# Kernel tuning notes

Hardware: AMD Instinct MI355X
Metric: run time of the kernel (lower is better)

Reference implementation:

```python
import jax, jax.numpy as jnp
import numpy as np
from jax import lax


def _conv(x, w, b):
    # x: [B,C,H,W], w: [O,I,3,3] (OIHW), SAME padding, stride 1
    y = lax.conv_general_dilated(x, w, (1, 1), 'SAME',
                                 dimension_numbers=('NCHW', 'OIHW', 'NCHW'))
    return y + b[None, :, None, None]


def _maxpool2(x):
    return lax.reduce_window(x, -jnp.inf, lax.max, (1, 1, 2, 2), (1, 1, 2, 2), 'VALID')


def setup_inputs() -> dict:
    key = jax.random.key(0)
    ks = iter(jax.random.split(key, 40))

    def conv_w(o, i):
        std = np.sqrt(2.0 / (9.0 * o)).astype(np.float32)  # kaiming as in _initialize_weights
        return jax.random.normal(next(ks), (o, i, 3, 3), jnp.float32) * std

    def lin_w(o, i):
        return jax.random.normal(next(ks), (o, i), jnp.float32) * 0.01

    inp = {
        'x': jax.random.normal(next(ks), (64, 3, 64, 64), jnp.float32),
        'y': jax.random.randint(next(ks), (64,), 0, 1000, dtype=jnp.int32),
        'b_table': jax.random.randint(next(ks), (1000, 128), 0, 512, dtype=jnp.int32),
        'cw0': conv_w(64, 3),    'cb0': jnp.zeros((64,), jnp.float32),
        'cw1': conv_w(128, 64),  'cb1': jnp.zeros((128,), jnp.float32),
        'cw2a': conv_w(256, 128), 'cb2a': jnp.zeros((256,), jnp.float32),
        'cw2b': conv_w(256, 256), 'cb2b': jnp.zeros((256,), jnp.float32),
        'cw3a': conv_w(512, 256), 'cb3a': jnp.zeros((512,), jnp.float32),
        'cw3b': conv_w(512, 512), 'cb3b': jnp.zeros((512,), jnp.float32),
        'cw4a': conv_w(512, 512), 'cb4a': jnp.zeros((512,), jnp.float32),
        'cw4b': conv_w(512, 512), 'cb4b': jnp.zeros((512,), jnp.float32),
        'fw1': lin_w(4096, 2048), 'fb1': jnp.zeros((4096,), jnp.float32),
        'fw2': lin_w(4096, 4096), 'fb2': jnp.zeros((4096,), jnp.float32),
        'fw3': lin_w(1000, 4096), 'fb3': jnp.zeros((1000,), jnp.float32),
    }
    return inp


def reference(x, y, b_table, cw0, cb0, cw1, cb1, cw2a, cb2a, cw2b, cb2b,
              cw3a, cb3a, cw3b, cb3b, cw4a, cb4a, cw4b, cb4b,
              fw1, fb1, fw2, fb2, fw3, fb3):
    B = x.shape[0]
    relu = jax.nn.relu
    # block0 (single conv, relu applied in forward)
    h = relu(_conv(x, cw0, cb0))
    h = _maxpool2(h)                       # 32x32
    # block1
    h = relu(_conv(h, cw1, cb1))
    h = _maxpool2(h)                       # 16x16
    # block2: conv, relu, conv (trailing relu stripped, applied in forward)
    h = relu(_conv(relu(_conv(h, cw2a, cb2a)), cw2b, cb2b))
    h = _maxpool2(h)                       # 8x8
    # block3
    h = relu(_conv(relu(_conv(h, cw3a, cb3a)), cw3b, cb3b))
    h = _maxpool2(h)                       # h==64 path: pool3 -> 4x4
    # block4
    h = relu(_conv(relu(_conv(h, cw4a, cb4a)), cw4b, cb4b))  # [B,512,4,4]

    # ---- engram channel masking (gather + sort + scatter) ----
    ranking = jnp.sort(b_table[y], axis=-1)            # [B, engram_number] channel ids
    mask = jnp.zeros((B, 512), h.dtype).at[jnp.arange(B)[:, None], ranking].set(1.0)
    h = h * mask[:, :, None, None]

    h = _maxpool2(h)                       # [B,512,2,2]
    h = h.reshape(B, -1)                   # [B,2048]
    # classifier (dropout = identity in eval mode)
    h = relu(h @ fw1.T + fb1)
    h = relu(h @ fw2.T + fb2)
    return h @ fw3.T + fb3                 # [B,1000]
```

## Files before the change

kernel.cpp:

```cpp
#include <hip/hip_runtime.h>
#include <hip/hip_bf16.h>
#include <cstddef>

typedef __attribute__((ext_vector_type(8))) short short8;
typedef __attribute__((ext_vector_type(4))) float fx4;
typedef __attribute__((ext_vector_type(4))) unsigned short us4;
typedef __attribute__((ext_vector_type(8))) unsigned short us8;

constexpr int BATCH = 64;

static __device__ __forceinline__ unsigned short f2bf(float x) {
    __hip_bfloat16 h = __float2bfloat16(x);
    return *reinterpret_cast<unsigned short*>(&h);
}

__global__ __launch_bounds__(256)
void conv0_kernel(const float* __restrict__ x, const float* __restrict__ w,
                  const float* __restrict__ bias, unsigned short* __restrict__ out)
{
    __shared__ float ins[3][18][19];
    const int tid  = threadIdx.x;
    const int lane = tid & 63;
    const int wv   = __builtin_amdgcn_readfirstlane(tid >> 6);
    const int img  = blockIdx.x >> 4;
    const int tile = blockIdx.x & 15;
    const int ty0  = (tile >> 2) * 16, tx0 = (tile & 3) * 16;
    const int py0  = (lane >> 3) * 2,  px0 = (lane & 7) * 2;
    const int co0  = wv * 16;

    for (int t = tid; t < 3*18*18; t += 256) {
        int xx = t % 18, yy = (t/18) % 18, ci = t/(18*18);
        int gy = ty0 + yy - 1, gx = tx0 + xx - 1;
        float v = 0.f;
        if (gy >= 0 && gy < 64 && gx >= 0 && gx < 64)
            v = x[((img*3 + ci)*64 + gy)*64 + gx];
        ins[ci][yy][xx] = v;
    }
    __syncthreads();

    float acc[16][4];
    #pragma unroll
    for (int j = 0; j < 16; j++)
        #pragma unroll
        for (int r = 0; r < 4; r++) acc[j][r] = 0.f;

    #pragma unroll
    for (int ci = 0; ci < 3; ci++) {
        float p[4][4];
        #pragma unroll
        for (int dy = 0; dy < 4; dy++)
            #pragma unroll
            for (int dx = 0; dx < 4; dx++)
                p[dy][dx] = ins[ci][py0+dy][px0+dx];
        #pragma unroll
        for (int j = 0; j < 16; j++) {
            const float* wp = w + ((co0+j)*3 + ci)*9;
            float w0=wp[0],w1=wp[1],w2=wp[2],w3=wp[3],w4=wp[4],
                  w5=wp[5],w6=wp[6],w7=wp[7],w8=wp[8];
            #pragma unroll
            for (int oy = 0; oy < 2; oy++)
                #pragma unroll
                for (int ox = 0; ox < 2; ox++)
                    acc[j][oy*2+ox] +=
                        p[oy+0][ox+0]*w0 + p[oy+0][ox+1]*w1 + p[oy+0][ox+2]*w2 +
                        p[oy+1][ox+0]*w3 + p[oy+1][ox+1]*w4 + p[oy+1][ox+2]*w5 +
                        p[oy+2][ox+0]*w6 + p[oy+2][ox+1]*w7 + p[oy+2][ox+2]*w8;
        }
    }

    us8 v0, v1;
    #pragma unroll
    for (int j = 0; j < 16; j++) {
        float m = fmaxf(fmaxf(acc[j][0], acc[j][1]), fmaxf(acc[j][2], acc[j][3]));
        unsigned short u = f2bf(fmaxf(m + bias[co0+j], 0.f));
        if (j < 8) v0[j] = u; else v1[j-8] = u;
    }
    int oy = (ty0+py0) >> 1, ox = (tx0+px0) >> 1;
    unsigned short* o = &out[((size_t)(img*32+oy)*32 + ox)*64 + co0];
    *(us8*)(o)     = v0;
    *(us8*)(o + 8) = v1;
}

struct PPAll {
    const float* src[7];
    unsigned long long dstoff[7];
    int cin[7];
    int cout[7];
    int end[7];
};

__global__ __launch_bounds__(256)
void prepack(PPAll a, unsigned short* __restrict__ wpbase)
{
    int t = blockIdx.x*256 + threadIdx.x;
    if (t >= 1024000) return;
    int l = 0;
    while (t >= a.end[l]) l++;
    int start = (l == 0) ? 0 : a.end[l-1];
    int local = t - start;
    int cin = a.cin[l], cout = a.cout[l];
    int co = local / cin, ci = local % cin;
    const float* s = a.src[l] + (size_t)local * 9;
    unsigned short* d = wpbase + a.dstoff[l];
    int kct = cin >> 5;
    #pragma unroll
    for (int k = 0; k < 9; k++)
        d[((size_t)(k*kct + (ci >> 5))*cout + co)*32 + (ci & 31)] = f2bf(s[k]);
}

template<int CIN, int COUT, int H, int CW, int SW, int P, int KS, bool POOL>
__global__ __launch_bounds__(256)
void conv_mfma(const unsigned short* __restrict__ in, const unsigned short* __restrict__ wp,
               const float* __restrict__ bias, void* __restrict__ outp)
{
    constexpr int RY  = (P == 1) ? 8 : 4;
    constexpr int HY  = RY + 2, HX = RY + 2;
    constexpr int KCT = CIN / 32;
    constexpr int KC  = KCT / KS;
    constexpr int REG = (P == 1) ? (H/8)*(H/8) : 1;
    constexpr int LP  = 40;
    static_assert(CW * SW == 4, "4 waves");

    __shared__ unsigned short ins[SW][P][HY][HX][LP];

    const int tid  = threadIdx.x;
    const int lane = tid & 63;
    const int wv   = __builtin_amdgcn_readfirstlane(tid >> 6);
    const int quad = lane >> 4;
    const int nn   = lane & 15;
    const int cg   = wv % CW;
    const int sg   = wv / CW;
    const int co0  = (blockIdx.y * CW + cg) * 64;
    const int ks   = (KS > 1) ? (int)blockIdx.z : 0;

    auto decode = [&](int rg, int& img, int& y0, int& x0) {
        if constexpr (P == 1) {
            img = rg / REG;
            int rs = rg % REG;
            constexpr int RXN = (P == 1) ? (H/8) : 1;
            y0 = (rs / RXN) * 8;
            x0 = (rs % RXN) * 8;
        } else {
            img = rg * 4; y0 = 0; x0 = 0;
        }
    };

    int w_img, w_y0, w_x0;
    decode(blockIdx.x * SW + sg, w_img, w_y0, w_x0);

    fx4 acc[4][4];
    #pragma unroll
    for (int mf = 0; mf < 4; mf++)
        #pragma unroll
        for (int nf = 0; nf < 4; nf++) {
            fx4 z = {0.f, 0.f, 0.f, 0.f};
            acc[mf][nf] = z;
        }

    #pragma unroll 1
    for (int kc = 0; kc < KC; kc++) {
        const int ci0 = (ks*KC + kc) * 32;
        __syncthreads();
        constexpr int U = SW*P*HY*HX*4;
        for (int u = tid; u < U; u += 256) {
            int q   = u & 3;
            int pix = u >> 2;
            int xx  = pix % HX;
            int yy  = (pix / HX) % HY;
            int pp  = (pix / (HX*HY)) % P;
            int ss  = pix / (HX*HY*P);
            int s_img, s_y0, s_x0;
            decode(blockIdx.x * SW + ss, s_img, s_y0, s_x0);
            int gy = s_y0 + yy - 1, gx = s_x0 + xx - 1;
            int imgp = s_img + ((P == 1) ? 0 : pp);
            us8 v;
            #pragma unroll
            for (int e = 0; e < 8; e++) v[e] = 0;
            if (gy >= 0 && gy < H && gx >= 0 && gx < H)
                v = *(const us8*)&in[(((size_t)imgp*H + gy)*H + gx)*CIN + ci0 + q*8];
            *(us8*)&ins[ss][pp][yy][xx][q*8] = v;
        }
        __syncthreads();

        for (int tap = 0; tap < 9; tap++) {
            const int dy = tap / 3, dx = tap % 3;
            const unsigned short* wb =
                wp + ((size_t)(tap*KCT + ks*KC + kc)*COUT + co0 + nn)*32 + quad*8;
            short8 a[4];
            #pragma unroll
            for (int mf = 0; mf < 4; mf++)
                a[mf] = *(const short8*)(wb + (size_t)mf*16*32);
            short8 b[4];
            #pragma unroll
            for (int nf = 0; nf < 4; nf++) {
                int pp, py, px;
                if constexpr (P == 1) { pp = 0;  py = (nf>>1)*4 + (nn>>2); px = (nf&1)*4 + (nn&3); }
                else                  { pp = nf; py = (nn>>2);             px = (nn&3); }
                b[nf] = *(const short8*)&ins[sg][pp][py+dy][px+dx][quad*8];
            }
            #pragma unroll
            for (int mf = 0; mf < 4; mf++)
                #pragma unroll
                for (int nf = 0; nf < 4; nf++)
                    acc[mf][nf] = __builtin_amdgcn_mfma_f32_16x16x32_bf16(
                        a[mf], b[nf], acc[mf][nf], 0, 0, 0);
        }
    }

    if constexpr (KS > 1) {
        float* part = (float*)outp;
        constexpr size_t NPIX = (size_t)BATCH * H * H;
        #pragma unroll
        for (int mf = 0; mf < 4; mf++)
            #pragma unroll
            for (int nf = 0; nf < 4; nf++) {
                int img, py, px;
                if constexpr (P == 1) { img = w_img;      py = w_y0 + (nf>>1)*4 + (nn>>2); px = w_x0 + (nf&1)*4 + (nn&3); }
                else                  { img = w_img + nf; py = (nn>>2);                    px = (nn&3); }
                size_t npix = (size_t)img*H*H + py*H + px;
                size_t idx  = ((size_t)ks*NPIX + npix)*COUT + co0 + mf*16 + quad*4;
                *(fx4*)&part[idx] = acc[mf][nf];
            }
    } else if constexpr (POOL) {
        unsigned short* out = (unsigned short*)outp;
        constexpr int HO = H/2;
        #pragma unroll
        for (int mf = 0; mf < 4; mf++) {
            fx4 b4 = *(const fx4*)&bias[co0 + mf*16 + quad*4];
            #pragma unroll
            for (int nf = 0; nf < 4; nf++) {
                us4 o;
                #pragma unroll
                for (int r = 0; r < 4; r++) {
                    float v = acc[mf][nf][r];
                    v = fmaxf(v, __shfl_xor(v, 1));
                    v = fmaxf(v, __shfl_xor(v, 4));
                    o[r] = f2bf(fmaxf(v + b4[r], 0.f));
                }
                if ((nn & 5) == 0) {
                    int py = w_y0 + (nf>>1)*4 + (nn>>2);
                    int px = w_x0 + (nf&1)*4 + (nn&3);
                    size_t idx = (((size_t)w_img*HO + (py>>1))*HO + (px>>1))*COUT
                               + co0 + mf*16 + quad*4;
                    *(us4*)&out[idx] = o;
                }
            }
        }
    } else {
        unsigned short* out = (unsigned short*)outp;
        #pragma unroll
        for (int mf = 0; mf < 4; mf++) {
            fx4 b4 = *(const fx4*)&bias[co0 + mf*16 + quad*4];
            #pragma unroll
            for (int nf = 0; nf < 4; nf++) {
                us4 o;
                #pragma unroll
                for (int r = 0; r < 4; r++)
                    o[r] = f2bf(fmaxf(acc[mf][nf][r] + b4[r], 0.f));
                int py = w_y0 + (nf>>1)*4 + (nn>>2);
                int px = w_x0 + (nf&1)*4 + (nn&3);
                size_t idx = (((size_t)w_img*H + py)*H + px)*COUT + co0 + mf*16 + quad*4;
                *(us4*)&out[idx] = o;
            }
        }
    }
}

template<int KS, int NPIX, int CO>
__global__ __launch_bounds__(256)
void combine_nhwc(const float* __restrict__ part, const float* __restrict__ bias,
                  unsigned short* __restrict__ out)
{
    constexpr int C4 = CO/4;
    int t = blockIdx.x*256 + threadIdx.x;
    if (t >= NPIX*C4) return;
    int c4 = t % C4, pix = t / C4;
    fx4 s = *(const fx4*)&bias[c4*4];
    #pragma unroll
    for (int k = 0; k < KS; k++)
        s += *(const fx4*)&part[((size_t)k*NPIX + pix)*CO + c4*4];
    us4 o;
    #pragma unroll
    for (int r = 0; r < 4; r++) o[r] = f2bf(fmaxf(s[r], 0.f));
    *(us4*)&out[(size_t)pix*CO + c4*4] = o;
}

template<int KS, int HI, int CO>
__global__ __launch_bounds__(256)
void combine_pool(const float* __restrict__ part, const float* __restrict__ bias,
                  unsigned short* __restrict__ out)
{
    constexpr int HO = HI/2, C4 = CO/4;
    constexpr size_t NPIX = (size_t)BATCH*HI*HI;
    int t = blockIdx.x*256 + threadIdx.x;
    if (t >= BATCH*HO*HO*C4) return;
    int c4 = t % C4;
    int r  = t / C4;
    int xo = r % HO, yo = (r/HO) % HO, img = r/(HO*HO);
    fx4 m = {-1e30f, -1e30f, -1e30f, -1e30f};
    #pragma unroll
    for (int iy = 0; iy < 2; iy++)
        #pragma unroll
        for (int ix = 0; ix < 2; ix++) {
            size_t pix = (size_t)img*HI*HI + (2*yo+iy)*HI + (2*xo+ix);
            fx4 s = {0.f,0.f,0.f,0.f};
            #pragma unroll
            for (int k = 0; k < KS; k++)
                s += *(const fx4*)&part[((size_t)k*NPIX + pix)*CO + c4*4];
            #pragma unroll
            for (int e = 0; e < 4; e++) m[e] = fmaxf(m[e], s[e]);
        }
    fx4 b4 = *(const fx4*)&bias[c4*4];
    us4 o;
    #pragma unroll
    for (int e = 0; e < 4; e++) o[e] = f2bf(fmaxf(m[e] + b4[e], 0.f));
    *(us4*)&out[((size_t)(img*HO+yo)*HO + xo)*CO + c4*4] = o;
}

__global__ __launch_bounds__(256)
void combine4b(const float* __restrict__ part, const float* __restrict__ bias,
               const float* __restrict__ mask, unsigned short* __restrict__ X0)
{
    int t = blockIdx.x*256 + threadIdx.x;
    if (t >= BATCH*512) return;
    int b = t / 512, c = t % 512;
    float s[16];
    #pragma unroll
    for (int p = 0; p < 16; p++) s[p] = 0.f;
    #pragma unroll
    for (int k = 0; k < 8; k++)
        #pragma unroll
        for (int p = 0; p < 16; p++)
            s[p] += part[((size_t)k*1024 + b*16 + p)*512 + c];
    float mk = mask[b*512 + c], bb = bias[c];
    us4 o;
    #pragma unroll
    for (int py = 0; py < 2; py++)
        #pragma unroll
        for (int px = 0; px < 2; px++) {
            float m = fmaxf(fmaxf(s[(2*py)*4 + 2*px],     s[(2*py)*4 + 2*px+1]),
                            fmaxf(s[(2*py+1)*4 + 2*px],   s[(2*py+1)*4 + 2*px+1]));
            o[py*2+px] = f2bf(mk * fmaxf(m + bb, 0.f));
        }
    *(us4*)&X0[(size_t)b*2048 + c*4] = o;
}

__global__ void build_mask(const int* __restrict__ y, const int* __restrict__ btab,
                           float* __restrict__ mask)
{
    __shared__ float m[512];
    int b = blockIdx.x;
    int t = threadIdx.x;
    for (int i = t; i < 512; i += 128) m[i] = 0.f;
    __syncthreads();
    int cls = y[b];
    int idx = btab[cls*128 + t];
    m[idx] = 1.0f;
    __syncthreads();
    for (int i = t; i < 512; i += 128) mask[b*512 + i] = m[i];
}

template<int K, int NP, int NREAL, int KSO>
__global__ __launch_bounds__(256)
void fc_mfma(const unsigned short* __restrict__ X, const float* __restrict__ W,
             float* __restrict__ P)
{
    constexpr int KW = K / (KSO*4);
    constexpr int NI = KW / 32;
    __shared__ alignas(16) unsigned short XL[4][64][40];
    __shared__ alignas(16) float R[64][68];

    const int tid  = threadIdx.x;
    const int lane = tid & 63;
    const int wv   = __builtin_amdgcn_readfirstlane(tid >> 6);
    const int quad = lane >> 4;
    const int nn   = lane & 15;
    const int c0   = blockIdx.x * 64;
    const int ksb  = blockIdx.y;
    const int k0   = (ksb*4 + wv) * KW;

    fx4 acc[4][4];
    #pragma unroll
    for (int mf = 0; mf < 4; mf++)
        #pragma unroll
        for (int nf = 0; nf < 4; nf++) {
            fx4 z = {0.f,0.f,0.f,0.f};
            acc[mf][nf] = z;
        }

    #pragma unroll
    for (int kc = 0; kc < NI; kc++) {
        const int kw = k0 + kc*32;
        const unsigned short* xp = X + (size_t)lane*K + kw;
        us8 x0 = *(const us8*)(xp);
        us8 x1 = *(const us8*)(xp + 8);
        us8 x2 = *(const us8*)(xp + 16);
        us8 x3 = *(const us8*)(xp + 24);
        *(us8*)&XL[wv][lane][0]  = x0;
        *(us8*)&XL[wv][lane][8]  = x1;
        *(us8*)&XL[wv][lane][16] = x2;
        *(us8*)&XL[wv][lane][24] = x3;
        short8 b[4];
        #pragma unroll
        for (int nf = 0; nf < 4; nf++) {
            int c = c0 + nf*16 + nn;
            if (c > NREAL-1) c = NREAL-1;
            const float* wp = W + (size_t)c*K + kw + quad*8;
            float4 f0 = *(const float4*)(wp);
            float4 f1 = *(const float4*)(wp + 4);
            short8 t;
            t[0] = (short)f2bf(f0.x); t[1] = (short)f2bf(f0.y);
            t[2] = (short)f2bf(f0.z); t[3] = (short)f2bf(f0.w);
            t[4] = (short)f2bf(f1.x); t[5] = (short)f2bf(f1.y);
            t[6] = (short)f2bf(f1.z); t[7] = (short)f2bf(f1.w);
            b[nf] = t;
        }
        short8 a[4];
        #pragma unroll
        for (int mf = 0; mf < 4; mf++)
            a[mf] = *(const short8*)&XL[wv][mf*16 + nn][quad*8];
        #pragma unroll
        for (int mf = 0; mf < 4; mf++)
            #pragma unroll
            for (int nf = 0; nf < 4; nf++)
                acc[mf][nf] = __builtin_amdgcn_mfma_f32_16x16x32_bf16(
                    a[mf], b[nf], acc[mf][nf], 0, 0, 0);
    }

    for (int ww = 0; ww < 4; ww++) {
        __syncthreads();
        if (wv == ww) {
            #pragma unroll
            for (int mf = 0; mf < 4; mf++)
                #pragma unroll
                for (int nf = 0; nf < 4; nf++) {
                    int n = nf*16 + nn;
                    #pragma unroll
                    for (int r = 0; r < 4; r++) {
                        int m = mf*16 + quad*4 + r;
                        float v = acc[mf][nf][r];
                        if (ww) v += R[m][n];
                        R[m][n] = v;
                    }
                }
        }
    }
    __syncthreads();
    {
        int m  = tid >> 2;
        int n0 = (tid & 3) * 16;
        float* dst = P + ((size_t)ksb*64 + m)*NP + c0 + n0;
        #pragma unroll
        for (int j = 0; j < 4; j++) {
            fx4 v = *(const fx4*)&R[m][n0 + j*4];
            *(fx4*)(dst + j*4) = v;
        }
    }
}

template<int N, int KS>
__global__ __launch_bounds__(256)
void fc_combine_bf16(const float* __restrict__ P, const float* __restrict__ bias,
                     unsigned short* __restrict__ Xo)
{
    int t = blockIdx.x*256 + threadIdx.x;
    if (t >= 64*(N/4)) return;
    int c4 = t % (N/4);
    int b  = t / (N/4);
    fx4 s = *(const fx4*)&bias[c4*4];
    #pragma unroll
    for (int ks = 0; ks < KS; ks++)
        s += *(const fx4*)&P[((size_t)ks*64 + b)*N + c4*4];
    us4 o;
    #pragma unroll
    for (int r = 0; r < 4; r++) o[r] = f2bf(fmaxf(s[r], 0.f));
    *(us4*)&Xo[(size_t)b*N + c4*4] = o;
}

__global__ __launch_bounds__(256)
void fc3_combine(const float* __restrict__ P, const float* __restrict__ bias,
                 float* __restrict__ out)
{
    int t = blockIdx.x*256 + threadIdx.x;
    if (t >= 64*1000) return;
    int b = t / 1000, c = t % 1000;
    float s = bias[c];
    #pragma unroll
    for (int ks = 0; ks < 16; ks++)
        s += P[((size_t)ks*64 + b)*1024 + c];
    out[t] = s;
}

extern "C" void kernel_launch(void* const* d_in, const int* in_sizes, int n_in,
                              void* d_out, int out_size, void* d_ws, size_t ws_size,
                              hipStream_t stream)
{
    const float* x    = (const float*)d_in[0];
    const int*   y    = (const int*)  d_in[1];
    const int*   btab = (const int*)  d_in[2];
    const float* cw0  = (const float*)d_in[3];  const float* cb0  = (const float*)d_in[4];
    const float* cw1  = (const float*)d_in[5];  const float* cb1  = (const float*)d_in[6];
    const float* cw2a = (const float*)d_in[7];  const float* cb2a = (const float*)d_in[8];
    const float* cw2b = (const float*)d_in[9];  const float* cb2b = (const float*)d_in[10];
    const float* cw3a = (const float*)d_in[11]; const float* cb3a = (const float*)d_in[12];
    const float* cw3b = (const float*)d_in[13]; const float* cb3b = (const float*)d_in[14];
    const float* cw4a = (const float*)d_in[15]; const float* cb4a = (const float*)d_in[16];
    const float* cw4b = (const float*)d_in[17]; const float* cb4b = (const float*)d_in[18];
    const float* fw1  = (const float*)d_in[19]; const float* fb1  = (const float*)d_in[20];
    const float* fw2  = (const float*)d_in[21]; const float* fb2  = (const float*)d_in[22];
    const float* fw3  = (const float*)d_in[23]; const float* fb3  = (const float*)d_in[24];
    (void)in_sizes; (void)n_in; (void)out_size; (void)ws_size;

    float* ws = (float*)d_ws;
    unsigned short* ActA = (unsigned short*)(ws);
    unsigned short* ActB = (unsigned short*)(ws + 2097152);
    float*          Pp   = ws + 3145728;
    unsigned short* Wp   = (unsigned short*)(ws + 7340032);
    float*          M    = ws + 11948032;
    unsigned short* X0   = (unsigned short*)(ws + 11980800);
    unsigned short* X1   = (unsigned short*)(ws + 12046336);
    unsigned short* X2   = (unsigned short*)(ws + 12177408);

    PPAll pa;
    const float* srcs[7] = {cw1, cw2a, cw2b, cw3a, cw3b, cw4a, cw4b};
    const unsigned long long doffs[7] = {0, 73728, 368640, 958464, 2138112, 4497408, 6856704};
    const int cins[7]  = {64, 128, 256, 256, 512, 512, 512};
    const int couts[7] = {128, 256, 256, 512, 512, 512, 512};
    const int ends[7]  = {8192, 40960, 106496, 237568, 499712, 761856, 1024000};
    for (int i = 0; i < 7; i++) {
        pa.src[i] = srcs[i]; pa.dstoff[i] = doffs[i];
        pa.cin[i] = cins[i]; pa.cout[i] = couts[i]; pa.end[i] = ends[i];
    }
    prepack<<<4000, 256, 0, stream>>>(pa, Wp);

    conv0_kernel<<<1024, 256, 0, stream>>>(x, cw0, cb0, ActA);
    conv_mfma<64,128,32,2,2,1,1,true><<<dim3(512,1,1),256,0,stream>>>(ActA, Wp+0, cb1, ActB);
    conv_mfma<128,256,16,4,1,1,1,false><<<dim3(256,1,1),256,0,stream>>>(ActB, Wp+73728, cb2a, ActA);
    conv_mfma<256,256,16,4,1,1,1,true><<<dim3(256,1,1),256,0,stream>>>(ActA, Wp+368640, cb2b, ActB);
    conv_mfma<256,512,8,2,2,1,2,false><<<dim3(32,4,2),256,0,stream>>>(ActB, Wp+958464, cb3a, Pp);
    combine_nhwc<2, 4096, 512><<<2048,256,0,stream>>>(Pp, cb3a, ActA);
    conv_mfma<512,512,8,2,2,1,2,false><<<dim3(32,4,2),256,0,stream>>>(ActA, Wp+2138112, cb3b, Pp);
    combine_pool<2, 8, 512><<<512,256,0,stream>>>(Pp, cb3b, ActB);
    conv_mfma<512,512,4,2,2,4,8,false><<<dim3(8,4,8),256,0,stream>>>(ActB, Wp+4497408, cb4a, Pp);
    combine_nhwc<8, 1024, 512><<<512,256,0,stream>>>(Pp, cb4a, ActA);
    build_mask<<<64,128,0,stream>>>(y, btab, M);
    conv_mfma<512,512,4,2,2,4,8,false><<<dim3(8,4,8),256,0,stream>>>(ActA, Wp+6856704, cb4b, Pp);
    combine4b<<<128,256,0,stream>>>(Pp, cb4b, M, X0);
    fc_mfma<2048,4096,4096,4><<<dim3(64,4),256,0,stream>>>(X0, fw1, Pp);
    fc_combine_bf16<4096,4><<<256,256,0,stream>>>(Pp, fb1, X1);
    fc_mfma<4096,4096,4096,8><<<dim3(64,8),256,0,stream>>>(X1, fw2, Pp);
    fc_combine_bf16<4096,8><<<256,256,0,stream>>>(Pp, fb2, X2);
    fc_mfma<4096,1024,1000,16><<<dim3(16,16),256,0,stream>>>(X2, fw3, Pp);
    fc3_combine<<<250,256,0,stream>>>(Pp, fb3, (float*)d_out);
}
```

Baseline: 625.0 us.

## Stage whole per-split input halo in LDS once and raise split-K across convs and FCs

The conv kernel now loads the full input-channel slice of its split into shared memory once, with a padded stride. The previous version reloaded a 32-channel halo, with two barriers, on every K-chunk. This removes most per-chunk synchronization. The mid-network convs (block2, block3, block4) and fc1/fc3 move to larger split-K with smaller channel tiles per block to raise block counts, which adds extra combine kernels for block2 and larger partial buffers. Larger LDS use per block and more partial-sum traffic are the costs, and the workspace offsets shift to make room.

```diff
diff --git a/kernel.cpp b/kernel.cpp
--- a/kernel.cpp
+++ b/kernel.cpp
@@ -109,19 +109,21 @@
 }
 
 template<int CIN, int COUT, int H, int CW, int SW, int P, int KS, bool POOL>
-__global__ __launch_bounds__(256)
+__global__ __launch_bounds__(256, 2)
 void conv_mfma(const unsigned short* __restrict__ in, const unsigned short* __restrict__ wp,
                const float* __restrict__ bias, void* __restrict__ outp)
 {
-    constexpr int RY  = (P == 1) ? 8 : 4;
-    constexpr int HY  = RY + 2, HX = RY + 2;
-    constexpr int KCT = CIN / 32;
-    constexpr int KC  = KCT / KS;
-    constexpr int REG = (P == 1) ? (H/8)*(H/8) : 1;
-    constexpr int LP  = 40;
+    constexpr int RY   = (P == 1) ? 8 : 4;
+    constexpr int HY   = RY + 2, HX = RY + 2;
+    constexpr int KCT  = CIN / 32;
+    constexpr int CINS = CIN / KS;
+    constexpr int KC   = CINS / 32;
+    constexpr int PADW = (CINS == 128) ? 24 : 8;
+    constexpr int STR  = CINS + PADW;
+    constexpr int REG  = (P == 1) ? (H/8)*(H/8) : 1;
     static_assert(CW * SW == 4, "4 waves");
 
-    __shared__ unsigned short ins[SW][P][HY][HX][LP];
+    __shared__ unsigned short ins[SW][P][HY][HX][STR];
 
     const int tid  = threadIdx.x;
     const int lane = tid & 63;
@@ -148,23 +150,11 @@
     int w_img, w_y0, w_x0;
     decode(blockIdx.x * SW + sg, w_img, w_y0, w_x0);
 
-    fx4 acc[4][4];
-    #pragma unroll
-    for (int mf = 0; mf < 4; mf++)
-        #pragma unroll
-        for (int nf = 0; nf < 4; nf++) {
-            fx4 z = {0.f, 0.f, 0.f, 0.f};
-            acc[mf][nf] = z;
-        }
-
-    #pragma unroll 1
-    for (int kc = 0; kc < KC; kc++) {
-        const int ci0 = (ks*KC + kc) * 32;
-        __syncthreads();
-        constexpr int U = SW*P*HY*HX*4;
-        for (int u = tid; u < U; u += 256) {
-            int q   = u & 3;
-            int pix = u >> 2;
+    {
+        constexpr int E = SW*P*HY*HX*(CINS/8);
+        for (int u = tid; u < E; u += 256) {
+            int q   = u % (CINS/8);
+            int pix = u / (CINS/8);
             int xx  = pix % HX;
             int yy  = (pix / HX) % HY;
             int pp  = (pix / (HX*HY)) % P;
@@ -177,11 +167,24 @@
             #pragma unroll
             for (int e = 0; e < 8; e++) v[e] = 0;
             if (gy >= 0 && gy < H && gx >= 0 && gx < H)
-                v = *(const us8*)&in[(((size_t)imgp*H + gy)*H + gx)*CIN + ci0 + q*8];
+                v = *(const us8*)&in[(((size_t)imgp*H + gy)*H + gx)*CIN + ks*CINS + q*8];
             *(us8*)&ins[ss][pp][yy][xx][q*8] = v;
         }
-        __syncthreads();
-
+    }
+    __syncthreads();
+
+    fx4 acc[4][4];
+    #pragma unroll
+    for (int mf = 0; mf < 4; mf++)
+        #pragma unroll
+        for (int nf = 0; nf < 4; nf++) {
+            fx4 z = {0.f, 0.f, 0.f, 0.f};
+            acc[mf][nf] = z;
+        }
+
+    #pragma unroll 1
+    for (int kc = 0; kc < KC; kc++) {
+        #pragma unroll 3
         for (int tap = 0; tap < 9; tap++) {
             const int dy = tap / 3, dx = tap % 3;
             const unsigned short* wb =
@@ -196,7 +199,7 @@
                 int pp, py, px;
                 if constexpr (P == 1) { pp = 0;  py = (nf>>1)*4 + (nn>>2); px = (nf&1)*4 + (nn&3); }
                 else                  { pp = nf; py = (nn>>2);             px = (nn&3); }
-                b[nf] = *(const short8*)&ins[sg][pp][py+dy][px+dx][quad*8];
+                b[nf] = *(const short8*)&ins[sg][pp][py+dy][px+dx][kc*32 + quad*8];
             }
             #pragma unroll
             for (int mf = 0; mf < 4; mf++)
@@ -328,7 +331,7 @@
     #pragma unroll
     for (int p = 0; p < 16; p++) s[p] = 0.f;
     #pragma unroll
-    for (int k = 0; k < 8; k++)
+    for (int k = 0; k < 16; k++)
         #pragma unroll
         for (int p = 0; p < 16; p++)
             s[p] += part[((size_t)k*1024 + b*16 + p)*512 + c];
@@ -486,7 +489,7 @@
     int b = t / 1000, c = t % 1000;
     float s = bias[c];
     #pragma unroll
-    for (int ks = 0; ks < 16; ks++)
+    for (int ks = 0; ks < 32; ks++)
         s += P[((size_t)ks*64 + b)*1024 + c];
     out[t] = s;
 }
@@ -515,11 +518,11 @@
     unsigned short* ActA = (unsigned short*)(ws);
     unsigned short* ActB = (unsigned short*)(ws + 2097152);
     float*          Pp   = ws + 3145728;
-    unsigned short* Wp   = (unsigned short*)(ws + 7340032);
-    float*          M    = ws + 11948032;
-    unsigned short* X0   = (unsigned short*)(ws + 11980800);
-    unsigned short* X1   = (unsigned short*)(ws + 12046336);
-    unsigned short* X2   = (unsigned short*)(ws + 12177408);
+    unsigned short* Wp   = (unsigned short*)(ws + 11534336);
+    float*          M    = ws + 16142336;
+    unsigned short* X0   = (unsigned short*)(ws + 16175104);
+    unsigned short* X1   = (unsigned short*)(ws + 16240640);
+    unsigned short* X2   = (unsigned short*)(ws + 16371712);
 
     PPAll pa;
     const float* srcs[7] = {cw1, cw2a, cw2b, cw3a, cw3b, cw4a, cw4b};
@@ -535,21 +538,23 @@
 
     conv0_kernel<<<1024, 256, 0, stream>>>(x, cw0, cb0, ActA);
     conv_mfma<64,128,32,2,2,1,1,true><<<dim3(512,1,1),256,0,stream>>>(ActA, Wp+0, cb1, ActB);
-    conv_mfma<128,256,16,4,1,1,1,false><<<dim3(256,1,1),256,0,stream>>>(ActB, Wp+73728, cb2a, ActA);
-    conv_mfma<256,256,16,4,1,1,1,true><<<dim3(256,1,1),256,0,stream>>>(ActA, Wp+368640, cb2b, ActB);
-    conv_mfma<256,512,8,2,2,1,2,false><<<dim3(32,4,2),256,0,stream>>>(ActB, Wp+958464, cb3a, Pp);
-    combine_nhwc<2, 4096, 512><<<2048,256,0,stream>>>(Pp, cb3a, ActA);
-    conv_mfma<512,512,8,2,2,1,2,false><<<dim3(32,4,2),256,0,stream>>>(ActA, Wp+2138112, cb3b, Pp);
-    combine_pool<2, 8, 512><<<512,256,0,stream>>>(Pp, cb3b, ActB);
-    conv_mfma<512,512,4,2,2,4,8,false><<<dim3(8,4,8),256,0,stream>>>(ActB, Wp+4497408, cb4a, Pp);
-    combine_nhwc<8, 1024, 512><<<512,256,0,stream>>>(Pp, cb4a, ActA);
+    conv_mfma<128,256,16,2,2,1,2,false><<<dim3(128,2,2),256,0,stream>>>(ActB, Wp+73728, cb2a, Pp);
+    combine_nhwc<2, 16384, 256><<<4096,256,0,stream>>>(Pp, cb2a, ActA);
+    conv_mfma<256,256,16,2,2,1,2,false><<<dim3(128,2,2),256,0,stream>>>(ActA, Wp+368640, cb2b, Pp);
+    combine_pool<2, 16, 256><<<1024,256,0,stream>>>(Pp, cb2b, ActB);
+    conv_mfma<256,512,8,4,1,1,4,false><<<dim3(64,2,4),256,0,stream>>>(ActB, Wp+958464, cb3a, Pp);
+    combine_nhwc<4, 4096, 512><<<2048,256,0,stream>>>(Pp, cb3a, ActA);
+    conv_mfma<512,512,8,4,1,1,4,false><<<dim3(64,2,4),256,0,stream>>>(ActA, Wp+2138112, cb3b, Pp);
+    combine_pool<4, 8, 512><<<512,256,0,stream>>>(Pp, cb3b, ActB);
+    conv_mfma<512,512,4,4,1,4,16,false><<<dim3(16,2,16),256,0,stream>>>(ActB, Wp+4497408, cb4a, Pp);
+    combine_nhwc<16, 1024, 512><<<512,256,0,stream>>>(Pp, cb4a, ActA);
     build_mask<<<64,128,0,stream>>>(y, btab, M);
-    conv_mfma<512,512,4,2,2,4,8,false><<<dim3(8,4,8),256,0,stream>>>(ActA, Wp+6856704, cb4b, Pp);
+    conv_mfma<512,512,4,4,1,4,16,false><<<dim3(16,2,16),256,0,stream>>>(ActA, Wp+6856704, cb4b, Pp);
     combine4b<<<128,256,0,stream>>>(Pp, cb4b, M, X0);
-    fc_mfma<2048,4096,4096,4><<<dim3(64,4),256,0,stream>>>(X0, fw1, Pp);
-    fc_combine_bf16<4096,4><<<256,256,0,stream>>>(Pp, fb1, X1);
+    fc_mfma<2048,4096,4096,8><<<dim3(64,8),256,0,stream>>>(X0, fw1, Pp);
+    fc_combine_bf16<4096,8><<<256,256,0,stream>>>(Pp, fb1, X1);
     fc_mfma<4096,4096,4096,8><<<dim3(64,8),256,0,stream>>>(X1, fw2, Pp);
     fc_combine_bf16<4096,8><<<256,256,0,stream>>>(Pp, fb2, X2);
-    fc_mfma<4096,1024,1000,16><<<dim3(16,16),256,0,stream>>>(X2, fw3, Pp);
+    fc_mfma<4096,1024,1000,32><<<dim3(16,32),256,0,stream>>>(X2, fw3, Pp);
     fc3_combine<<<250,256,0,stream>>>(Pp, fb3, (float*)d_out);
 }
```

New measurement: 516.3 us. 17.4% less time.
